# Kernel tuning notes

Measured on AMD Instinct MI355X. Metric: run time of the kernel, lower is better.

Reference implementation:

```python
import jax, jax.numpy as jnp
import numpy as np

N = 1_000_000   # atoms
E = 4_000_000   # directed edges
G = 1024        # graphs in batch
IN = 64         # input atom feature size
H = 32          # hidden_feats
OUT = 1         # out_feats
EPS = 1e-5


def setup_inputs() -> dict:
    key = jax.random.key(0)
    ks = jax.random.split(key, 16)
    def w(k, shape):
        fan_in = shape[0]
        return jax.random.normal(k, shape, jnp.float32) / np.sqrt(fan_in)
    inp = {}
    inp['feats'] = jax.random.normal(ks[0], (N, IN), jnp.float32)
    inp['src'] = jax.random.randint(ks[1], (E,), 0, N, dtype=jnp.int32)
    inp['dst'] = jax.random.randint(ks[2], (E,), 0, N, dtype=jnp.int32)
    inp['gid'] = jnp.sort(jax.random.randint(ks[3], (N,), 0, G, dtype=jnp.int32))
    # input MLP
    inp['w0'] = w(ks[4], (IN, H)); inp['b0'] = jnp.zeros((H,), jnp.float32)
    inp['g0'] = jnp.ones((H,), jnp.float32); inp['be0'] = jnp.zeros((H,), jnp.float32)
    # block 1: GraphConv + node MLP
    inp['wc1'] = w(ks[5], (H, H)); inp['bc1'] = jnp.zeros((H,), jnp.float32)
    inp['w1'] = w(ks[6], (H, H)); inp['b1'] = jnp.zeros((H,), jnp.float32)
    inp['g1'] = jnp.ones((H,), jnp.float32); inp['be1'] = jnp.zeros((H,), jnp.float32)
    # block 2
    inp['wc2'] = w(ks[7], (H, H)); inp['bc2'] = jnp.zeros((H,), jnp.float32)
    inp['w2'] = w(ks[8], (H, H)); inp['b2'] = jnp.zeros((H,), jnp.float32)
    inp['g2'] = jnp.ones((H,), jnp.float32); inp['be2'] = jnp.zeros((H,), jnp.float32)
    # output head
    inp['wout'] = w(ks[9], (H, OUT)); inp['bout'] = jnp.zeros((OUT,), jnp.float32)
    return inp


def _ln(x, g, b):
    mu = jnp.mean(x, axis=-1, keepdims=True)
    var = jnp.mean(jnp.square(x - mu), axis=-1, keepdims=True)
    return (x - mu) * jax.lax.rsqrt(var + EPS) * g + b


def reference(feats, src, dst, gid,
              w0, b0, g0, be0,
              wc1, bc1, w1, b1, g1, be1,
              wc2, bc2, w2, b2, g2, be2,
              wout, bout):
    elu = jax.nn.elu
    ones_e = jnp.ones((E,), jnp.float32)
    deg_out = jax.ops.segment_sum(ones_e, src, num_segments=N)
    deg_in = jax.ops.segment_sum(ones_e, dst, num_segments=N)
    # dgl norm='both': zero-degree nodes get norm 0
    ns = jnp.where(deg_out > 0, jax.lax.rsqrt(jnp.maximum(deg_out, 1.0)), 0.0)[:, None]
    nd = jnp.where(deg_in > 0, jax.lax.rsqrt(jnp.maximum(deg_in, 1.0)), 0.0)[:, None]

    # input node MLP: Linear -> LayerNorm -> (Dropout p=0) -> ELU
    h = elu(_ln(feats @ w0 + b0, g0, be0))

    for wc, bc, w, b, g, be in ((wc1, bc1, w1, b1, g1, be1),
                                (wc2, bc2, w2, b2, g2, be2)):
        # GraphConv: gather-normalize-scatter then dense transform + ELU
        m = jax.ops.segment_sum((h * ns)[src], dst, num_segments=N) * nd
        h = elu(m @ wc + bc)
        # node MLP block
        h = elu(_ln(h @ w + b, g, be))

    # output head: Linear -> ELU
    h = elu(h @ wout + bout)                 # [N, OUT]
    # dgl.sum_nodes: per-graph readout
    return jax.ops.segment_sum(h, gid, num_segments=G)   # [G, OUT]
```

## Files before the change

### kernel.cpp

```cpp
#include <hip/hip_runtime.h>
#include <math.h>

#define N_ATOMS 1000000
#define N_EDGES 4000000
#define N_GRAPHS 1024
#define IN_F 64
#define HID 32
#define LN_EPS 1e-5f
#define NB 1024
#define PB 512
#define CHUNK ((N_EDGES + PB - 1) / PB)
#define NBUCK_USED 977

typedef unsigned int uint;
typedef unsigned short ushort;

__device__ __forceinline__ float elu_f(float x) {
    return x > 0.0f ? x : expm1f(x);
}
__device__ __forceinline__ uint f2bf(float x) {
    uint u = __float_as_uint(x);
    return (u + 0x7fffu + ((u >> 16) & 1u)) >> 16;
}

__global__ __launch_bounds__(256) void hist2(const int* __restrict__ src,
                                             const int* __restrict__ dst,
                                             int* __restrict__ Hs,
                                             int* __restrict__ Hd) {
    __shared__ int hs[NB], hd[NB];
    int blk = blockIdx.x, tid = threadIdx.x;
    for (int i = tid; i < NB; i += 256) { hs[i] = 0; hd[i] = 0; }
    __syncthreads();
    int e0 = blk * CHUNK, e1 = min(N_EDGES, e0 + CHUNK);
    for (int e = e0 + tid; e < e1; e += 256) {
        atomicAdd(&hs[src[e] >> 10], 1);
        atomicAdd(&hd[dst[e] >> 10], 1);
    }
    __syncthreads();
    for (int i = tid; i < NB; i += 256) {
        Hs[blk * NB + i] = hs[i];
        Hd[blk * NB + i] = hd[i];
    }
}

__global__ __launch_bounds__(256) void col_scan(int* __restrict__ H,
                                                int* __restrict__ btot) {
    __shared__ int lds[256];
    int b = blockIdx.x, tid = threadIdx.x;
    int v0 = H[(2 * tid) * NB + b];
    int v1 = H[(2 * tid + 1) * NB + b];
    lds[tid] = v0 + v1;
    __syncthreads();
    for (int off = 1; off < 256; off <<= 1) {
        int t = (tid >= off) ? lds[tid - off] : 0;
        __syncthreads();
        lds[tid] += t;
        __syncthreads();
    }
    int excl = (tid > 0) ? lds[tid - 1] : 0;
    H[(2 * tid) * NB + b] = excl;
    H[(2 * tid + 1) * NB + b] = excl + v0;
    if (tid == 255) btot[b] = excl + v0 + v1;
}

__global__ __launch_bounds__(256) void bucket_scan(const int* __restrict__ btot_d,
                                                   int* __restrict__ bbase_d,
                                                   const int* __restrict__ btot_s,
                                                   int* __restrict__ bbase_s) {
    __shared__ int lds[256];
    const int* in = (blockIdx.x == 0) ? btot_d : btot_s;
    int* out = (blockIdx.x == 0) ? bbase_d : bbase_s;
    int tid = threadIdx.x;
    int v[4]; int s = 0;
#pragma unroll
    for (int q = 0; q < 4; ++q) { v[q] = in[tid * 4 + q]; s += v[q]; }
    lds[tid] = s;
    __syncthreads();
    for (int off = 1; off < 256; off <<= 1) {
        int t = (tid >= off) ? lds[tid - off] : 0;
        __syncthreads();
        lds[tid] += t;
        __syncthreads();
    }
    int run = (tid > 0) ? lds[tid - 1] : 0;
#pragma unroll
    for (int q = 0; q < 4; ++q) { out[tid * 4 + q] = run; run += v[q]; }
    if (tid == 255) out[NB] = run;
}

__global__ __launch_bounds__(256) void scatter_dst(const int* __restrict__ src,
                                                   const int* __restrict__ dst,
                                                   const int* __restrict__ Hd,
                                                   const int* __restrict__ bbase_d,
                                                   int2* __restrict__ pedge) {
    __shared__ int cur[NB];
    int blk = blockIdx.x, tid = threadIdx.x;
    for (int i = tid; i < NB; i += 256) cur[i] = bbase_d[i] + Hd[blk * NB + i];
    __syncthreads();
    int e0 = blk * CHUNK, e1 = min(N_EDGES, e0 + CHUNK);
    for (int e = e0 + tid; e < e1; e += 256) {
        int d = dst[e], s = src[e];
        int pos = atomicAdd(&cur[d >> 10], 1);
        pedge[pos] = make_int2(d, s);
    }
}

__global__ __launch_bounds__(256) void scatter_src(const int* __restrict__ src,
                                                   const int* __restrict__ Hs,
                                                   const int* __restrict__ bbase_s,
                                                   int* __restrict__ psrc) {
    __shared__ int cur[NB];
    int blk = blockIdx.x, tid = threadIdx.x;
    for (int i = tid; i < NB; i += 256) cur[i] = bbase_s[i] + Hs[blk * NB + i];
    __syncthreads();
    int e0 = blk * CHUNK, e1 = min(N_EDGES, e0 + CHUNK);
    for (int e = e0 + tid; e < e1; e += 256) {
        int s = src[e];
        int pos = atomicAdd(&cur[s >> 10], 1);
        psrc[pos] = s;
    }
}

__global__ __launch_bounds__(256) void bucket_csr(const int2* __restrict__ pedge,
                                                  const int* __restrict__ bbase_d,
                                                  int* __restrict__ eidx,
                                                  int* __restrict__ offs,
                                                  float* __restrict__ nd) {
    __shared__ int deg[NB];
    __shared__ int cur[NB];
    __shared__ int lds[256];
    int b = blockIdx.x, tid = threadIdx.x;
    int nbase = b << 10;
    if (nbase > N_ATOMS) return;
    int ebase = bbase_d[b], eend = bbase_d[b + 1];
    for (int i = tid; i < NB; i += 256) deg[i] = 0;
    __syncthreads();
    for (int i = ebase + tid; i < eend; i += 256)
        atomicAdd(&deg[pedge[i].x & (NB - 1)], 1);
    __syncthreads();
    int v[4]; int s = 0;
#pragma unroll
    for (int q = 0; q < 4; ++q) { v[q] = deg[tid * 4 + q]; s += v[q]; }
    lds[tid] = s;
    __syncthreads();
    for (int off = 1; off < 256; off <<= 1) {
        int t = (tid >= off) ? lds[tid - off] : 0;
        __syncthreads();
        lds[tid] += t;
        __syncthreads();
    }
    int run = (tid > 0) ? lds[tid - 1] : 0;
#pragma unroll
    for (int q = 0; q < 4; ++q) {
        int l = tid * 4 + q;
        cur[l] = run;
        int node = nbase + l;
        if (node <= N_ATOMS) {
            offs[node] = ebase + run;
            if (node < N_ATOMS) nd[node] = v[q] > 0 ? rsqrtf((float)v[q]) : 0.0f;
        }
        run += v[q];
    }
    __syncthreads();
    for (int i = ebase + tid; i < eend; i += 256) {
        int2 ed = pedge[i];
        int p = atomicAdd(&cur[ed.x & (NB - 1)], 1);
        eidx[ebase + p] = ed.y;
    }
}

__global__ __launch_bounds__(256) void bucket_ns(const int* __restrict__ psrc,
                                                 const int* __restrict__ bbase_s,
                                                 float* __restrict__ ns) {
    __shared__ int deg[NB];
    int b = blockIdx.x, tid = threadIdx.x;
    int nbase = b << 10;
    if (nbase >= N_ATOMS) return;
    int ebase = bbase_s[b], eend = bbase_s[b + 1];
    for (int i = tid; i < NB; i += 256) deg[i] = 0;
    __syncthreads();
    for (int i = ebase + tid; i < eend; i += 256)
        atomicAdd(&deg[psrc[i] & (NB - 1)], 1);
    __syncthreads();
    for (int l = tid; l < NB; l += 256) {
        int node = nbase + l;
        if (node < N_ATOMS) {
            int c = deg[l];
            ns[node] = c > 0 ? rsqrtf((float)c) : 0.0f;
        }
    }
}

__global__ __launch_bounds__(256) void input_mlp(const float* __restrict__ feats,
                                                 const float* __restrict__ w0,
                                                 const float* __restrict__ b0,
                                                 const float* __restrict__ g0,
                                                 const float* __restrict__ be0,
                                                 const float* __restrict__ ns,
                                                 ushort* __restrict__ hs) {
    __shared__ float sf[256 * 65];
    __shared__ float sw[IN_F * HID];
    int base = blockIdx.x * 256;
    int tid = threadIdx.x;

    for (int i = tid; i < IN_F * HID; i += 256) sw[i] = w0[i];

    int nrows = min(256, N_ATOMS - base);
    for (int i = tid; i < nrows * IN_F; i += 256) {
        int r = i >> 6, c = i & 63;
        sf[r * 65 + c] = feats[(size_t)base * IN_F + i];
    }
    __syncthreads();
    if (tid >= nrows) return;

    float acc[HID];
#pragma unroll
    for (int j = 0; j < HID; ++j) acc[j] = b0[j];

    const float* frow = &sf[tid * 65];
#pragma unroll 4
    for (int k = 0; k < IN_F; ++k) {
        float f = frow[k];
#pragma unroll
        for (int j = 0; j < HID; ++j) acc[j] += f * sw[k * HID + j];
    }

    float mu = 0.0f;
#pragma unroll
    for (int j = 0; j < HID; ++j) mu += acc[j];
    mu *= (1.0f / HID);
    float var = 0.0f;
#pragma unroll
    for (int j = 0; j < HID; ++j) { float d = acc[j] - mu; var += d * d; }
    var *= (1.0f / HID);
    float rs = rsqrtf(var + LN_EPS);

    float os = ns[base + tid];
#pragma unroll
    for (int j = 0; j < HID; ++j)
        acc[j] = elu_f((acc[j] - mu) * rs * g0[j] + be0[j]) * os;

    uint words[HID / 2];
#pragma unroll
    for (int q = 0; q < HID / 2; ++q)
        words[q] = f2bf(acc[2 * q]) | (f2bf(acc[2 * q + 1]) << 16);
    uint4* hv = (uint4*)&hs[(size_t)(base + tid) * HID];
#pragma unroll
    for (int q = 0; q < 4; ++q)
        hv[q] = make_uint4(words[4 * q], words[4 * q + 1], words[4 * q + 2], words[4 * q + 3]);
}

__global__ __launch_bounds__(256) void conv_node(const ushort* __restrict__ hin,
                                                 const int* __restrict__ offs,
                                                 const int* __restrict__ eidx,
                                                 const float* __restrict__ nd,
                                                 const float* __restrict__ wc,
                                                 const float* __restrict__ bc,
                                                 const float* __restrict__ w,
                                                 const float* __restrict__ b,
                                                 const float* __restrict__ g,
                                                 const float* __restrict__ be,
                                                 const float* __restrict__ ns_out,
                                                 ushort* __restrict__ hout) {
    __shared__ float swc[HID * HID];
    __shared__ float sw[HID * HID];
    int tid = threadIdx.x;
    for (int i = tid; i < HID * HID; i += 256) { swc[i] = wc[i]; sw[i] = w[i]; }
    __syncthreads();

    int node = blockIdx.x * 256 + tid;
    if (node >= N_ATOMS) return;

    int s0 = offs[node], s1 = offs[node + 1];
    float acc[HID];
#pragma unroll
    for (int j = 0; j < HID; ++j) acc[j] = 0.0f;

    for (int i = s0; i < s1; ++i) {
        int s = eidx[i];
        const uint4* hr = (const uint4*)(hin + (size_t)s * HID);
#pragma unroll
        for (int q = 0; q < 4; ++q) {
            uint4 u = hr[q];
            uint vv[4] = {u.x, u.y, u.z, u.w};
#pragma unroll
            for (int r = 0; r < 4; ++r) {
                acc[q * 8 + r * 2]     += __uint_as_float(vv[r] << 16);
                acc[q * 8 + r * 2 + 1] += __uint_as_float(vv[r] & 0xffff0000u);
            }
        }
    }

    float scale = nd[node];
    float t1[HID];
#pragma unroll
    for (int j = 0; j < HID; ++j) t1[j] = bc[j];
#pragma unroll 4
    for (int k = 0; k < HID; ++k) {
        float f = acc[k] * scale;
#pragma unroll
        for (int j = 0; j < HID; ++j) t1[j] += f * swc[k * HID + j];
    }
#pragma unroll
    for (int j = 0; j < HID; ++j) t1[j] = elu_f(t1[j]);

    float t2[HID];
#pragma unroll
    for (int j = 0; j < HID; ++j) t2[j] = b[j];
#pragma unroll 4
    for (int k = 0; k < HID; ++k) {
        float f = t1[k];
#pragma unroll
        for (int j = 0; j < HID; ++j) t2[j] += f * sw[k * HID + j];
    }

    float mu = 0.0f;
#pragma unroll
    for (int j = 0; j < HID; ++j) mu += t2[j];
    mu *= (1.0f / HID);
    float var = 0.0f;
#pragma unroll
    for (int j = 0; j < HID; ++j) { float d = t2[j] - mu; var += d * d; }
    var *= (1.0f / HID);
    float rs = rsqrtf(var + LN_EPS);

    float os = ns_out ? ns_out[node] : 1.0f;
#pragma unroll
    for (int j = 0; j < HID; ++j)
        t2[j] = elu_f((t2[j] - mu) * rs * g[j] + be[j]) * os;

    uint words[HID / 2];
#pragma unroll
    for (int q = 0; q < HID / 2; ++q)
        words[q] = f2bf(t2[2 * q]) | (f2bf(t2[2 * q + 1]) << 16);
    uint4* hv = (uint4*)&hout[(size_t)node * HID];
#pragma unroll
    for (int q = 0; q < 4; ++q)
        hv[q] = make_uint4(words[4 * q], words[4 * q + 1], words[4 * q + 2], words[4 * q + 3]);
}

__global__ __launch_bounds__(256) void readout(const ushort* __restrict__ h,
                                               const int* __restrict__ gid,
                                               const float* __restrict__ wout,
                                               const float* __restrict__ bout,
                                               float* __restrict__ out) {
    __shared__ float swout[HID];
    __shared__ float buckets[N_GRAPHS];
    __shared__ int s_gf, s_range;
    int base = blockIdx.x * 256;
    int tid = threadIdx.x;
    int nrows = min(256, N_ATOMS - base);

    if (tid < HID) swout[tid] = wout[tid];
    if (tid == 0) {
        int gf = gid[base];
        int gl = gid[base + nrows - 1];
        s_gf = gf;
        s_range = gl - gf + 1;
    }
    __syncthreads();
    int gf = s_gf, range = s_range;
    for (int i = tid; i < range; i += 256) buckets[i] = 0.0f;
    __syncthreads();

    if (tid < nrows) {
        int node = base + tid;
        const uint4* hv = (const uint4*)&h[(size_t)node * HID];
        float acc = bout[0];
#pragma unroll
        for (int q = 0; q < 4; ++q) {
            uint4 u = hv[q];
            uint vv[4] = {u.x, u.y, u.z, u.w};
#pragma unroll
            for (int r = 0; r < 4; ++r) {
                float lo = __uint_as_float(vv[r] << 16);
                float hi = __uint_as_float(vv[r] & 0xffff0000u);
                acc += lo * swout[q * 8 + r * 2] + hi * swout[q * 8 + r * 2 + 1];
            }
        }
        acc = elu_f(acc);
        atomicAdd(&buckets[gid[node] - gf], acc);
    }
    __syncthreads();
    for (int i = tid; i < range; i += 256) {
        float v = buckets[i];
        if (v != 0.0f) atomicAdd(&out[gf + i], v);
    }
}

extern "C" void kernel_launch(void* const* d_in, const int* in_sizes, int n_in,
                              void* d_out, int out_size, void* d_ws, size_t ws_size,
                              hipStream_t stream) {
    const float* feats = (const float*)d_in[0];
    const int* src = (const int*)d_in[1];
    const int* dst = (const int*)d_in[2];
    const int* gid = (const int*)d_in[3];
    const float* w0  = (const float*)d_in[4];
    const float* b0  = (const float*)d_in[5];
    const float* g0  = (const float*)d_in[6];
    const float* be0 = (const float*)d_in[7];
    const float* wc1 = (const float*)d_in[8];
    const float* bc1 = (const float*)d_in[9];
    const float* w1  = (const float*)d_in[10];
    const float* b1  = (const float*)d_in[11];
    const float* g1  = (const float*)d_in[12];
    const float* be1 = (const float*)d_in[13];
    const float* wc2 = (const float*)d_in[14];
    const float* bc2 = (const float*)d_in[15];
    const float* w2  = (const float*)d_in[16];
    const float* b2  = (const float*)d_in[17];
    const float* g2  = (const float*)d_in[18];
    const float* be2 = (const float*)d_in[19];
    const float* wout = (const float*)d_in[20];
    const float* bout = (const float*)d_in[21];
    float* out = (float*)d_out;

    char* ws = (char*)d_ws;
    ushort* h0    = (ushort*)(ws + 0);
    ushort* h1    = (ushort*)(ws + 64000000);
    int* offs     = (int*)(ws + 128000000);
    int* eidx     = (int*)(ws + 132000064);
    int2* pedge   = (int2*)(ws + 148000064);
    int* psrc     = (int*)(ws + 180000064);
    int* Hd       = (int*)(ws + 196000064);
    int* Hs       = (int*)(ws + 198100000);
    int* btot_d   = (int*)(ws + 200200000);
    int* btot_s   = (int*)(ws + 200204096);
    int* bbase_d  = (int*)(ws + 200208192);
    int* bbase_s  = (int*)(ws + 200212296);
    float* ns     = (float*)(ws + 200216396);
    float* nd     = (float*)(ws + 204216396);

    hipMemsetAsync(out, 0, (size_t)N_GRAPHS * sizeof(float), stream);

    int nb = (N_ATOMS + 255) / 256;

    hist2<<<PB, 256, 0, stream>>>(src, dst, Hs, Hd);
    col_scan<<<NB, 256, 0, stream>>>(Hd, btot_d);
    col_scan<<<NB, 256, 0, stream>>>(Hs, btot_s);
    bucket_scan<<<2, 256, 0, stream>>>(btot_d, bbase_d, btot_s, bbase_s);
    scatter_dst<<<PB, 256, 0, stream>>>(src, dst, Hd, bbase_d, pedge);
    scatter_src<<<PB, 256, 0, stream>>>(src, Hs, bbase_s, psrc);
    bucket_csr<<<NBUCK_USED, 256, 0, stream>>>(pedge, bbase_d, eidx, offs, nd);
    bucket_ns<<<NBUCK_USED, 256, 0, stream>>>(psrc, bbase_s, ns);

    input_mlp<<<nb, 256, 0, stream>>>(feats, w0, b0, g0, be0, ns, h0);

    conv_node<<<nb, 256, 0, stream>>>(h0, offs, eidx, nd, wc1, bc1, w1, b1, g1, be1, ns, h1);
    conv_node<<<nb, 256, 0, stream>>>(h1, offs, eidx, nd, wc2, bc2, w2, b2, g2, be2, nullptr, h0);

    readout<<<nb, 256, 0, stream>>>(h0, gid, wout, bout, out);
}
```

Before: 660.0 us.

## Replace CSR gather with per-bucket LDS atomic aggregation in conv

Removes the bucket_csr kernel and the per-node CSR. Each 1024-node destination bucket is now handled by one 512-thread block that accumulates neighbour features with float atomics into a padded LDS tile. The in-degree norm is derived from an LDS counter, and the dense transform, LayerNorm and ELU are then applied per node. This drops a sort pass and the offs/eidx traffic and keeps the scatter in LDS. The costs are about 140KB of LDS per block, which limits occupancy, heavy LDS atomic contention, and a summation order that is no longer deterministic.

```diff
diff --git a/kernel.cpp b/kernel.cpp
--- a/kernel.cpp
+++ b/kernel.cpp
@@ -11,6 +11,8 @@
 #define PB 512
 #define CHUNK ((N_EDGES + PB - 1) / PB)
 #define NBUCK_USED 977
+#define MPAD 33
+#define CONV_LDS_BYTES (NB * MPAD * 4 + NB * 4 + 2 * HID * HID * 4)
 
 typedef unsigned int uint;
 typedef unsigned short ushort;
@@ -118,54 +120,6 @@
         int s = src[e];
         int pos = atomicAdd(&cur[s >> 10], 1);
         psrc[pos] = s;
-    }
-}
-
-__global__ __launch_bounds__(256) void bucket_csr(const int2* __restrict__ pedge,
-                                                  const int* __restrict__ bbase_d,
-                                                  int* __restrict__ eidx,
-                                                  int* __restrict__ offs,
-                                                  float* __restrict__ nd) {
-    __shared__ int deg[NB];
-    __shared__ int cur[NB];
-    __shared__ int lds[256];
-    int b = blockIdx.x, tid = threadIdx.x;
-    int nbase = b << 10;
-    if (nbase > N_ATOMS) return;
-    int ebase = bbase_d[b], eend = bbase_d[b + 1];
-    for (int i = tid; i < NB; i += 256) deg[i] = 0;
-    __syncthreads();
-    for (int i = ebase + tid; i < eend; i += 256)
-        atomicAdd(&deg[pedge[i].x & (NB - 1)], 1);
-    __syncthreads();
-    int v[4]; int s = 0;
-#pragma unroll
-    for (int q = 0; q < 4; ++q) { v[q] = deg[tid * 4 + q]; s += v[q]; }
-    lds[tid] = s;
-    __syncthreads();
-    for (int off = 1; off < 256; off <<= 1) {
-        int t = (tid >= off) ? lds[tid - off] : 0;
-        __syncthreads();
-        lds[tid] += t;
-        __syncthreads();
-    }
-    int run = (tid > 0) ? lds[tid - 1] : 0;
-#pragma unroll
-    for (int q = 0; q < 4; ++q) {
-        int l = tid * 4 + q;
-        cur[l] = run;
-        int node = nbase + l;
-        if (node <= N_ATOMS) {
-            offs[node] = ebase + run;
-            if (node < N_ATOMS) nd[node] = v[q] > 0 ? rsqrtf((float)v[q]) : 0.0f;
-        }
-        run += v[q];
-    }
-    __syncthreads();
-    for (int i = ebase + tid; i < eend; i += 256) {
-        int2 ed = pedge[i];
-        int p = atomicAdd(&cur[ed.x & (NB - 1)], 1);
-        eidx[ebase + p] = ed.y;
     }
 }
 
@@ -250,93 +204,133 @@
         hv[q] = make_uint4(words[4 * q], words[4 * q + 1], words[4 * q + 2], words[4 * q + 3]);
 }
 
-__global__ __launch_bounds__(256) void conv_node(const ushort* __restrict__ hin,
-                                                 const int* __restrict__ offs,
-                                                 const int* __restrict__ eidx,
-                                                 const float* __restrict__ nd,
-                                                 const float* __restrict__ wc,
-                                                 const float* __restrict__ bc,
-                                                 const float* __restrict__ w,
-                                                 const float* __restrict__ b,
-                                                 const float* __restrict__ g,
-                                                 const float* __restrict__ be,
-                                                 const float* __restrict__ ns_out,
-                                                 ushort* __restrict__ hout) {
-    __shared__ float swc[HID * HID];
-    __shared__ float sw[HID * HID];
-    int tid = threadIdx.x;
-    for (int i = tid; i < HID * HID; i += 256) { swc[i] = wc[i]; sw[i] = w[i]; }
-    __syncthreads();
-
-    int node = blockIdx.x * 256 + tid;
-    if (node >= N_ATOMS) return;
-
-    int s0 = offs[node], s1 = offs[node + 1];
-    float acc[HID];
-#pragma unroll
-    for (int j = 0; j < HID; ++j) acc[j] = 0.0f;
-
-    for (int i = s0; i < s1; ++i) {
-        int s = eidx[i];
-        const uint4* hr = (const uint4*)(hin + (size_t)s * HID);
-#pragma unroll
-        for (int q = 0; q < 4; ++q) {
-            uint4 u = hr[q];
-            uint vv[4] = {u.x, u.y, u.z, u.w};
-#pragma unroll
-            for (int r = 0; r < 4; ++r) {
-                acc[q * 8 + r * 2]     += __uint_as_float(vv[r] << 16);
-                acc[q * 8 + r * 2 + 1] += __uint_as_float(vv[r] & 0xffff0000u);
-            }
-        }
-    }
-
-    float scale = nd[node];
-    float t1[HID];
-#pragma unroll
-    for (int j = 0; j < HID; ++j) t1[j] = bc[j];
+__global__ __launch_bounds__(512) void conv_lds(const ushort* __restrict__ hin,
+                                                const int2* __restrict__ pedge,
+                                                const int* __restrict__ bbase_d,
+                                                const float* __restrict__ wc,
+                                                const float* __restrict__ bc,
+                                                const float* __restrict__ w,
+                                                const float* __restrict__ b,
+                                                const float* __restrict__ g,
+                                                const float* __restrict__ be,
+                                                const float* __restrict__ ns_out,
+                                                ushort* __restrict__ hout) {
+    extern __shared__ char smem[];
+    float* sm  = (float*)smem;
+    int* sdeg  = (int*)(smem + NB * MPAD * 4);
+    float* swc = (float*)(smem + NB * MPAD * 4 + NB * 4);
+    float* sww = swc + HID * HID;
+
+    int bkt = blockIdx.x, tid = threadIdx.x;
+    int nbase = bkt << 10;
+    int ebase = bbase_d[bkt], eend = bbase_d[bkt + 1];
+
+    for (int i = tid; i < NB * MPAD; i += 512) sm[i] = 0.0f;
+    for (int i = tid; i < NB; i += 512) sdeg[i] = 0;
+    for (int i = tid; i < HID * HID; i += 512) { swc[i] = wc[i]; sww[i] = w[i]; }
+    __syncthreads();
+
+    int i0 = ebase + tid;
+    for (; i0 + 512 < eend; i0 += 1024) {
+        int2 ea = pedge[i0];
+        int2 eb = pedge[i0 + 512];
+        const uint4* ra = (const uint4*)(hin + (size_t)ea.y * HID);
+        const uint4* rb = (const uint4*)(hin + (size_t)eb.y * HID);
+        uint4 a0 = ra[0], a1 = ra[1], a2 = ra[2], a3 = ra[3];
+        uint4 b0 = rb[0], b1 = rb[1], b2 = rb[2], b3 = rb[3];
+        int la = ea.x & (NB - 1), lb = eb.x & (NB - 1);
+        atomicAdd(&sdeg[la], 1);
+        atomicAdd(&sdeg[lb], 1);
+        float* ma = &sm[la * MPAD];
+        float* mb = &sm[lb * MPAD];
+        uint va[16] = {a0.x, a0.y, a0.z, a0.w, a1.x, a1.y, a1.z, a1.w,
+                       a2.x, a2.y, a2.z, a2.w, a3.x, a3.y, a3.z, a3.w};
+        uint vb[16] = {b0.x, b0.y, b0.z, b0.w, b1.x, b1.y, b1.z, b1.w,
+                       b2.x, b2.y, b2.z, b2.w, b3.x, b3.y, b3.z, b3.w};
+#pragma unroll
+        for (int r = 0; r < 16; ++r) {
+            atomicAdd(ma + 2 * r,     __uint_as_float(va[r] << 16));
+            atomicAdd(ma + 2 * r + 1, __uint_as_float(va[r] & 0xffff0000u));
+        }
+#pragma unroll
+        for (int r = 0; r < 16; ++r) {
+            atomicAdd(mb + 2 * r,     __uint_as_float(vb[r] << 16));
+            atomicAdd(mb + 2 * r + 1, __uint_as_float(vb[r] & 0xffff0000u));
+        }
+    }
+    if (i0 < eend) {
+        int2 ea = pedge[i0];
+        const uint4* ra = (const uint4*)(hin + (size_t)ea.y * HID);
+        uint4 a0 = ra[0], a1 = ra[1], a2 = ra[2], a3 = ra[3];
+        int la = ea.x & (NB - 1);
+        atomicAdd(&sdeg[la], 1);
+        float* ma = &sm[la * MPAD];
+        uint va[16] = {a0.x, a0.y, a0.z, a0.w, a1.x, a1.y, a1.z, a1.w,
+                       a2.x, a2.y, a2.z, a2.w, a3.x, a3.y, a3.z, a3.w};
+#pragma unroll
+        for (int r = 0; r < 16; ++r) {
+            atomicAdd(ma + 2 * r,     __uint_as_float(va[r] << 16));
+            atomicAdd(ma + 2 * r + 1, __uint_as_float(va[r] & 0xffff0000u));
+        }
+    }
+    __syncthreads();
+
+#pragma unroll
+    for (int half = 0; half < 2; ++half) {
+        int l = tid + half * 512;
+        int node = nbase + l;
+        if (node >= N_ATOMS) continue;
+
+        int dg = sdeg[l];
+        float scale = dg > 0 ? rsqrtf((float)dg) : 0.0f;
+        const float* mr = &sm[l * MPAD];
+
+        float t1[HID];
+#pragma unroll
+        for (int j = 0; j < HID; ++j) t1[j] = bc[j];
 #pragma unroll 4
-    for (int k = 0; k < HID; ++k) {
-        float f = acc[k] * scale;
-#pragma unroll
-        for (int j = 0; j < HID; ++j) t1[j] += f * swc[k * HID + j];
-    }
-#pragma unroll
-    for (int j = 0; j < HID; ++j) t1[j] = elu_f(t1[j]);
-
-    float t2[HID];
-#pragma unroll
-    for (int j = 0; j < HID; ++j) t2[j] = b[j];
+        for (int k = 0; k < HID; ++k) {
+            float f = mr[k] * scale;
+#pragma unroll
+            for (int j = 0; j < HID; ++j) t1[j] += f * swc[k * HID + j];
+        }
+#pragma unroll
+        for (int j = 0; j < HID; ++j) t1[j] = elu_f(t1[j]);
+
+        float t2[HID];
+#pragma unroll
+        for (int j = 0; j < HID; ++j) t2[j] = b[j];
 #pragma unroll 4
-    for (int k = 0; k < HID; ++k) {
-        float f = t1[k];
-#pragma unroll
-        for (int j = 0; j < HID; ++j) t2[j] += f * sw[k * HID + j];
-    }
-
-    float mu = 0.0f;
-#pragma unroll
-    for (int j = 0; j < HID; ++j) mu += t2[j];
-    mu *= (1.0f / HID);
-    float var = 0.0f;
-#pragma unroll
-    for (int j = 0; j < HID; ++j) { float d = t2[j] - mu; var += d * d; }
-    var *= (1.0f / HID);
-    float rs = rsqrtf(var + LN_EPS);
-
-    float os = ns_out ? ns_out[node] : 1.0f;
-#pragma unroll
-    for (int j = 0; j < HID; ++j)
-        t2[j] = elu_f((t2[j] - mu) * rs * g[j] + be[j]) * os;
-
-    uint words[HID / 2];
-#pragma unroll
-    for (int q = 0; q < HID / 2; ++q)
-        words[q] = f2bf(t2[2 * q]) | (f2bf(t2[2 * q + 1]) << 16);
-    uint4* hv = (uint4*)&hout[(size_t)node * HID];
-#pragma unroll
-    for (int q = 0; q < 4; ++q)
-        hv[q] = make_uint4(words[4 * q], words[4 * q + 1], words[4 * q + 2], words[4 * q + 3]);
+        for (int k = 0; k < HID; ++k) {
+            float f = t1[k];
+#pragma unroll
+            for (int j = 0; j < HID; ++j) t2[j] += f * sww[k * HID + j];
+        }
+
+        float mu = 0.0f;
+#pragma unroll
+        for (int j = 0; j < HID; ++j) mu += t2[j];
+        mu *= (1.0f / HID);
+        float var = 0.0f;
+#pragma unroll
+        for (int j = 0; j < HID; ++j) { float d = t2[j] - mu; var += d * d; }
+        var *= (1.0f / HID);
+        float rs = rsqrtf(var + LN_EPS);
+
+        float os = ns_out ? ns_out[node] : 1.0f;
+#pragma unroll
+        for (int j = 0; j < HID; ++j)
+            t2[j] = elu_f((t2[j] - mu) * rs * g[j] + be[j]) * os;
+
+        uint words[HID / 2];
+#pragma unroll
+        for (int q = 0; q < HID / 2; ++q)
+            words[q] = f2bf(t2[2 * q]) | (f2bf(t2[2 * q + 1]) << 16);
+        uint4* hv = (uint4*)&hout[(size_t)node * HID];
+#pragma unroll
+        for (int q = 0; q < 4; ++q)
+            hv[q] = make_uint4(words[4 * q], words[4 * q + 1], words[4 * q + 2], words[4 * q + 3]);
+    }
 }
 
 __global__ __launch_bounds__(256) void readout(const ushort* __restrict__ h,
@@ -418,18 +412,15 @@
     char* ws = (char*)d_ws;
     ushort* h0    = (ushort*)(ws + 0);
     ushort* h1    = (ushort*)(ws + 64000000);
-    int* offs     = (int*)(ws + 128000000);
-    int* eidx     = (int*)(ws + 132000064);
-    int2* pedge   = (int2*)(ws + 148000064);
-    int* psrc     = (int*)(ws + 180000064);
-    int* Hd       = (int*)(ws + 196000064);
-    int* Hs       = (int*)(ws + 198100000);
-    int* btot_d   = (int*)(ws + 200200000);
-    int* btot_s   = (int*)(ws + 200204096);
-    int* bbase_d  = (int*)(ws + 200208192);
-    int* bbase_s  = (int*)(ws + 200212296);
-    float* ns     = (float*)(ws + 200216396);
-    float* nd     = (float*)(ws + 204216396);
+    int2* pedge   = (int2*)(ws + 128000000);
+    int* psrc     = (int*)(ws + 160000000);
+    int* Hd       = (int*)(ws + 176000000);
+    int* Hs       = (int*)(ws + 178097152);
+    int* btot_d   = (int*)(ws + 180194304);
+    int* btot_s   = (int*)(ws + 180198400);
+    int* bbase_d  = (int*)(ws + 180202496);
+    int* bbase_s  = (int*)(ws + 180206848);
+    float* ns     = (float*)(ws + 180211200);
 
     hipMemsetAsync(out, 0, (size_t)N_GRAPHS * sizeof(float), stream);
 
@@ -441,13 +432,16 @@
     bucket_scan<<<2, 256, 0, stream>>>(btot_d, bbase_d, btot_s, bbase_s);
     scatter_dst<<<PB, 256, 0, stream>>>(src, dst, Hd, bbase_d, pedge);
     scatter_src<<<PB, 256, 0, stream>>>(src, Hs, bbase_s, psrc);
-    bucket_csr<<<NBUCK_USED, 256, 0, stream>>>(pedge, bbase_d, eidx, offs, nd);
     bucket_ns<<<NBUCK_USED, 256, 0, stream>>>(psrc, bbase_s, ns);
 
     input_mlp<<<nb, 256, 0, stream>>>(feats, w0, b0, g0, be0, ns, h0);
 
-    conv_node<<<nb, 256, 0, stream>>>(h0, offs, eidx, nd, wc1, bc1, w1, b1, g1, be1, ns, h1);
-    conv_node<<<nb, 256, 0, stream>>>(h1, offs, eidx, nd, wc2, bc2, w2, b2, g2, be2, nullptr, h0);
+    hipFuncSetAttribute(reinterpret_cast<const void*>(conv_lds),
+                        hipFuncAttributeMaxDynamicSharedMemorySize, CONV_LDS_BYTES);
+    conv_lds<<<NBUCK_USED, 512, CONV_LDS_BYTES, stream>>>(h0, pedge, bbase_d,
+                                                          wc1, bc1, w1, b1, g1, be1, ns, h1);
+    conv_lds<<<NBUCK_USED, 512, CONV_LDS_BYTES, stream>>>(h1, pedge, bbase_d,
+                                                          wc2, bc2, w2, b2, g2, be2, nullptr, h0);
 
     readout<<<nb, 256, 0, stream>>>(h0, gid, wout, bout, out);
 }
```

Measured after the change: 2.034 ms. 208% more time.

## Split each node's conv across four lanes with shared-memory row exchange

Applied to the files above, without the earlier changes.

Rewrites the GraphConv+MLP kernel so four threads cooperate on each node, each gathering an 8-feature slice of the neighbour rows (unrolled by 4 edges). The matmul inputs are exchanged through padded shared memory, and LayerNorm statistics are reduced with lane shuffles. The in-degree norm is now computed from the CSR offsets instead of a stored array, so the nd buffer and its writes go away. This raises memory-level parallelism and cuts per-thread register pressure in the gather. The cost is more threads, an extra block sync and shared-memory traffic for the dense transforms.

```diff
diff --git a/kernel.cpp b/kernel.cpp
--- a/kernel.cpp
+++ b/kernel.cpp
@@ -22,6 +22,14 @@
     uint u = __float_as_uint(x);
     return (u + 0x7fffu + ((u >> 16) & 1u)) >> 16;
 }
+__device__ __forceinline__ void acc8(float* a, uint4 u) {
+    uint v[4] = {u.x, u.y, u.z, u.w};
+#pragma unroll
+    for (int r = 0; r < 4; ++r) {
+        a[2 * r]     += __uint_as_float(v[r] << 16);
+        a[2 * r + 1] += __uint_as_float(v[r] & 0xffff0000u);
+    }
+}
 
 __global__ __launch_bounds__(256) void hist2(const int* __restrict__ src,
                                              const int* __restrict__ dst,
@@ -124,8 +132,7 @@
 __global__ __launch_bounds__(256) void bucket_csr(const int2* __restrict__ pedge,
                                                   const int* __restrict__ bbase_d,
                                                   int* __restrict__ eidx,
-                                                  int* __restrict__ offs,
-                                                  float* __restrict__ nd) {
+                                                  int* __restrict__ offs) {
     __shared__ int deg[NB];
     __shared__ int cur[NB];
     __shared__ int lds[256];
@@ -155,10 +162,7 @@
         int l = tid * 4 + q;
         cur[l] = run;
         int node = nbase + l;
-        if (node <= N_ATOMS) {
-            offs[node] = ebase + run;
-            if (node < N_ATOMS) nd[node] = v[q] > 0 ? rsqrtf((float)v[q]) : 0.0f;
-        }
+        if (node <= N_ATOMS) offs[node] = ebase + run;
         run += v[q];
     }
     __syncthreads();
@@ -250,93 +254,98 @@
         hv[q] = make_uint4(words[4 * q], words[4 * q + 1], words[4 * q + 2], words[4 * q + 3]);
 }
 
-__global__ __launch_bounds__(256) void conv_node(const ushort* __restrict__ hin,
-                                                 const int* __restrict__ offs,
-                                                 const int* __restrict__ eidx,
-                                                 const float* __restrict__ nd,
-                                                 const float* __restrict__ wc,
-                                                 const float* __restrict__ bc,
-                                                 const float* __restrict__ w,
-                                                 const float* __restrict__ b,
-                                                 const float* __restrict__ g,
-                                                 const float* __restrict__ be,
-                                                 const float* __restrict__ ns_out,
-                                                 ushort* __restrict__ hout) {
+__global__ __launch_bounds__(256) void conv4(const ushort* __restrict__ hin,
+                                             const int* __restrict__ offs,
+                                             const int* __restrict__ eidx,
+                                             const float* __restrict__ wc,
+                                             const float* __restrict__ bc,
+                                             const float* __restrict__ w,
+                                             const float* __restrict__ b,
+                                             const float* __restrict__ g,
+                                             const float* __restrict__ be,
+                                             const float* __restrict__ ns_out,
+                                             ushort* __restrict__ hout) {
     __shared__ float swc[HID * HID];
-    __shared__ float sw[HID * HID];
+    __shared__ float sww[HID * HID];
+    __shared__ float sm[64 * 33];
     int tid = threadIdx.x;
-    for (int i = tid; i < HID * HID; i += 256) { swc[i] = wc[i]; sw[i] = w[i]; }
-    __syncthreads();
-
-    int node = blockIdx.x * 256 + tid;
-    if (node >= N_ATOMS) return;
-
-    int s0 = offs[node], s1 = offs[node + 1];
-    float acc[HID];
-#pragma unroll
-    for (int j = 0; j < HID; ++j) acc[j] = 0.0f;
-
-    for (int i = s0; i < s1; ++i) {
-        int s = eidx[i];
-        const uint4* hr = (const uint4*)(hin + (size_t)s * HID);
-#pragma unroll
-        for (int q = 0; q < 4; ++q) {
-            uint4 u = hr[q];
-            uint vv[4] = {u.x, u.y, u.z, u.w};
-#pragma unroll
-            for (int r = 0; r < 4; ++r) {
-                acc[q * 8 + r * 2]     += __uint_as_float(vv[r] << 16);
-                acc[q * 8 + r * 2 + 1] += __uint_as_float(vv[r] & 0xffff0000u);
-            }
-        }
-    }
-
-    float scale = nd[node];
-    float t1[HID];
-#pragma unroll
-    for (int j = 0; j < HID; ++j) t1[j] = bc[j];
-#pragma unroll 4
+    for (int i = tid; i < HID * HID; i += 256) { swc[i] = wc[i]; sww[i] = w[i]; }
+
+    int t = blockIdx.x * 256 + tid;
+    int row = t >> 2;
+    int l4 = (t & 3) * 8;
+    int lrow = tid >> 2;
+
+    float a[8] = {0.f, 0.f, 0.f, 0.f, 0.f, 0.f, 0.f, 0.f};
+    int s0 = offs[row], s1 = offs[row + 1];
+    int i = s0;
+    for (; i + 4 <= s1; i += 4) {
+        int e0 = eidx[i], e1 = eidx[i + 1], e2 = eidx[i + 2], e3 = eidx[i + 3];
+        uint4 r0 = *(const uint4*)(hin + (size_t)e0 * HID + l4);
+        uint4 r1 = *(const uint4*)(hin + (size_t)e1 * HID + l4);
+        uint4 r2 = *(const uint4*)(hin + (size_t)e2 * HID + l4);
+        uint4 r3 = *(const uint4*)(hin + (size_t)e3 * HID + l4);
+        acc8(a, r0); acc8(a, r1); acc8(a, r2); acc8(a, r3);
+    }
+    for (; i < s1; ++i) {
+        uint4 r0 = *(const uint4*)(hin + (size_t)eidx[i] * HID + l4);
+        acc8(a, r0);
+    }
+
+    float* myrow = &sm[lrow * 33];
+#pragma unroll
+    for (int jj = 0; jj < 8; ++jj) myrow[l4 + jj] = a[jj];
+    __syncthreads();
+
+    int deg = s1 - s0;
+    float scale = deg > 0 ? rsqrtf((float)deg) : 0.0f;
+
+    float t1[8];
+#pragma unroll
+    for (int jj = 0; jj < 8; ++jj) t1[jj] = bc[l4 + jj];
     for (int k = 0; k < HID; ++k) {
-        float f = acc[k] * scale;
-#pragma unroll
-        for (int j = 0; j < HID; ++j) t1[j] += f * swc[k * HID + j];
-    }
-#pragma unroll
-    for (int j = 0; j < HID; ++j) t1[j] = elu_f(t1[j]);
-
-    float t2[HID];
-#pragma unroll
-    for (int j = 0; j < HID; ++j) t2[j] = b[j];
-#pragma unroll 4
+        float f = myrow[k] * scale;
+#pragma unroll
+        for (int jj = 0; jj < 8; ++jj) t1[jj] += f * swc[k * HID + l4 + jj];
+    }
+#pragma unroll
+    for (int jj = 0; jj < 8; ++jj) t1[jj] = elu_f(t1[jj]);
+
+#pragma unroll
+    for (int jj = 0; jj < 8; ++jj) myrow[l4 + jj] = t1[jj];
+
+    float t2[8];
+#pragma unroll
+    for (int jj = 0; jj < 8; ++jj) t2[jj] = b[l4 + jj];
     for (int k = 0; k < HID; ++k) {
-        float f = t1[k];
-#pragma unroll
-        for (int j = 0; j < HID; ++j) t2[j] += f * sw[k * HID + j];
-    }
-
-    float mu = 0.0f;
-#pragma unroll
-    for (int j = 0; j < HID; ++j) mu += t2[j];
-    mu *= (1.0f / HID);
-    float var = 0.0f;
-#pragma unroll
-    for (int j = 0; j < HID; ++j) { float d = t2[j] - mu; var += d * d; }
-    var *= (1.0f / HID);
-    float rs = rsqrtf(var + LN_EPS);
-
-    float os = ns_out ? ns_out[node] : 1.0f;
-#pragma unroll
-    for (int j = 0; j < HID; ++j)
-        t2[j] = elu_f((t2[j] - mu) * rs * g[j] + be[j]) * os;
-
-    uint words[HID / 2];
-#pragma unroll
-    for (int q = 0; q < HID / 2; ++q)
-        words[q] = f2bf(t2[2 * q]) | (f2bf(t2[2 * q + 1]) << 16);
-    uint4* hv = (uint4*)&hout[(size_t)node * HID];
-#pragma unroll
-    for (int q = 0; q < 4; ++q)
-        hv[q] = make_uint4(words[4 * q], words[4 * q + 1], words[4 * q + 2], words[4 * q + 3]);
+        float f = myrow[k];
+#pragma unroll
+        for (int jj = 0; jj < 8; ++jj) t2[jj] += f * sww[k * HID + l4 + jj];
+    }
+
+    float s = 0.0f;
+#pragma unroll
+    for (int jj = 0; jj < 8; ++jj) s += t2[jj];
+    s += __shfl_xor(s, 1);
+    s += __shfl_xor(s, 2);
+    float mu = s * (1.0f / HID);
+    float v = 0.0f;
+#pragma unroll
+    for (int jj = 0; jj < 8; ++jj) { float d = t2[jj] - mu; v += d * d; }
+    v += __shfl_xor(v, 1);
+    v += __shfl_xor(v, 2);
+    float rs = rsqrtf(v * (1.0f / HID) + LN_EPS);
+
+    float os = ns_out ? ns_out[row] : 1.0f;
+#pragma unroll
+    for (int jj = 0; jj < 8; ++jj)
+        t2[jj] = elu_f((t2[jj] - mu) * rs * g[l4 + jj] + be[l4 + jj]) * os;
+
+    uint w0 = f2bf(t2[0]) | (f2bf(t2[1]) << 16);
+    uint w1 = f2bf(t2[2]) | (f2bf(t2[3]) << 16);
+    uint w2 = f2bf(t2[4]) | (f2bf(t2[5]) << 16);
+    uint w3 = f2bf(t2[6]) | (f2bf(t2[7]) << 16);
+    *(uint4*)(hout + (size_t)row * HID + l4) = make_uint4(w0, w1, w2, w3);
 }
 
 __global__ __launch_bounds__(256) void readout(const ushort* __restrict__ h,
@@ -420,20 +429,20 @@
     ushort* h1    = (ushort*)(ws + 64000000);
     int* offs     = (int*)(ws + 128000000);
     int* eidx     = (int*)(ws + 132000064);
-    int2* pedge   = (int2*)(ws + 148000064);
-    int* psrc     = (int*)(ws + 180000064);
-    int* Hd       = (int*)(ws + 196000064);
-    int* Hs       = (int*)(ws + 198100000);
-    int* btot_d   = (int*)(ws + 200200000);
-    int* btot_s   = (int*)(ws + 200204096);
-    int* bbase_d  = (int*)(ws + 200208192);
-    int* bbase_s  = (int*)(ws + 200212296);
-    float* ns     = (float*)(ws + 200216396);
-    float* nd     = (float*)(ws + 204216396);
+    float* ns     = (float*)(ws + 148000064);
+    int2* pedge   = (int2*)(ws + 152000064);
+    int* psrc     = (int*)(ws + 184000064);
+    int* Hd       = (int*)(ws + 200000064);
+    int* Hs       = (int*)(ws + 202097216);
+    int* btot_d   = (int*)(ws + 204194368);
+    int* btot_s   = (int*)(ws + 204198464);
+    int* bbase_d  = (int*)(ws + 204202560);
+    int* bbase_s  = (int*)(ws + 204207168);
 
     hipMemsetAsync(out, 0, (size_t)N_GRAPHS * sizeof(float), stream);
 
     int nb = (N_ATOMS + 255) / 256;
+    int cb = (N_ATOMS * 4) / 256;
 
     hist2<<<PB, 256, 0, stream>>>(src, dst, Hs, Hd);
     col_scan<<<NB, 256, 0, stream>>>(Hd, btot_d);
@@ -441,13 +450,13 @@
     bucket_scan<<<2, 256, 0, stream>>>(btot_d, bbase_d, btot_s, bbase_s);
     scatter_dst<<<PB, 256, 0, stream>>>(src, dst, Hd, bbase_d, pedge);
     scatter_src<<<PB, 256, 0, stream>>>(src, Hs, bbase_s, psrc);
-    bucket_csr<<<NBUCK_USED, 256, 0, stream>>>(pedge, bbase_d, eidx, offs, nd);
+    bucket_csr<<<NBUCK_USED, 256, 0, stream>>>(pedge, bbase_d, eidx, offs);
     bucket_ns<<<NBUCK_USED, 256, 0, stream>>>(psrc, bbase_s, ns);
 
     input_mlp<<<nb, 256, 0, stream>>>(feats, w0, b0, g0, be0, ns, h0);
 
-    conv_node<<<nb, 256, 0, stream>>>(h0, offs, eidx, nd, wc1, bc1, w1, b1, g1, be1, ns, h1);
-    conv_node<<<nb, 256, 0, stream>>>(h1, offs, eidx, nd, wc2, bc2, w2, b2, g2, be2, nullptr, h0);
+    conv4<<<cb, 256, 0, stream>>>(h0, offs, eidx, wc1, bc1, w1, b1, g1, be1, ns, h1);
+    conv4<<<cb, 256, 0, stream>>>(h1, offs, eidx, wc2, bc2, w2, b2, g2, be2, nullptr, h0);
 
     readout<<<nb, 256, 0, stream>>>(h0, gid, wout, bout, out);
 }
```

Result: slower. 1.398 ms (+111.8%).
